# Kernel optimization log

Measured on AMD Instinct MI355X. Metric: run time of the kernel, lower is better.

Reference implementation:

```python
import jax, jax.numpy as jnp
import numpy as np

B, N, HID = 4, 1024, 256
NH, DH = 8, 32          # heads, head dim (HID = NH*DH)
BH = 64                 # bias MLP hidden


def setup_inputs() -> dict:
    key = jax.random.key(0)
    ks = jax.random.split(key, 12)
    s = lambda fan_in: 1.0 / np.sqrt(fan_in)
    return {
        "h": jax.random.normal(ks[0], (B, N, HID), jnp.float32),
        "coord": jax.random.uniform(ks[1], (B, N), jnp.float32),
        "mask": jnp.ones((B, N), jnp.int32),
        # qkv / proj linear params (stored [in, out])
        "Wqkv": jax.random.normal(ks[2], (HID, 3 * HID), jnp.float32) * s(HID),
        "bqkv": jnp.zeros((3 * HID,), jnp.float32),
        "Wproj": jax.random.normal(ks[3], (HID, HID), jnp.float32) * s(HID),
        "bproj": jnp.zeros((HID,), jnp.float32),
        # layernorm
        "gamma": jnp.ones((HID,), jnp.float32),
        "beta": jnp.zeros((HID,), jnp.float32),
        # relative-bias MLP: Linear(1->BH), SiLU, Linear(BH->BH), SiLU, Linear(BH->NH)
        "Wb1": jax.random.normal(ks[4], (1, BH), jnp.float32),
        "bb1": jnp.zeros((BH,), jnp.float32),
        "Wb2": jax.random.normal(ks[5], (BH, BH), jnp.float32) * s(BH),
        "bb2": jnp.zeros((BH,), jnp.float32),
        "Wb3": jax.random.normal(ks[6], (BH, NH), jnp.float32) * s(BH),
        "bb3": jnp.zeros((NH,), jnp.float32),
    }


def _layernorm(x, gamma, beta, eps=1e-5):
    mu = jnp.mean(x, axis=-1, keepdims=True)
    var = jnp.mean((x - mu) ** 2, axis=-1, keepdims=True)
    return (x - mu) * jax.lax.rsqrt(var + eps) * gamma + beta


def reference(h, coord, mask, Wqkv, bqkv, Wproj, bproj, gamma, beta,
              Wb1, bb1, Wb2, bb2, Wb3, bb3):
    x = _layernorm(h, gamma, beta)                      # [B,N,HID]
    qkv = x @ Wqkv + bqkv                               # [B,N,3*HID]
    q, k, v = jnp.split(qkv, 3, axis=-1)
    # [B,N,HID] -> [B,NH,N,DH]
    reshape = lambda t: t.reshape(B, N, NH, DH).transpose(0, 2, 1, 3)
    q, k, v = reshape(q), reshape(k), reshape(v)

    attn = jnp.einsum("bhqd,bhkd->bhqk", q, k) / np.sqrt(DH).astype(np.float32)

    # pairwise coordinate differences and learned bias
    dcoord = coord[:, None, :] - coord[:, :, None]      # [B,N,N]
    t = dcoord[..., None]                               # [B,N,N,1]
    t = jax.nn.silu(t @ Wb1 + bb1)                      # [B,N,N,BH]
    t = jax.nn.silu(t @ Wb2 + bb2)                      # [B,N,N,BH]
    bias = (t @ Wb3 + bb3)                              # [B,N,N,NH]
    attn = attn + bias.transpose(0, 3, 1, 2)            # [B,NH,N,N]

    neg_inf = jnp.array(-jnp.inf, attn.dtype)
    attn = jnp.where(mask[:, None, None, :] == 0, neg_inf, attn)
    w = jax.nn.softmax(attn, axis=-1)

    out = jnp.einsum("bhqk,bhkd->bhqd", w, v)           # [B,NH,N,DH]
    out = out.transpose(0, 2, 1, 3).reshape(B, N, HID)
    out = out @ Wproj + bproj
    return h + out
```

## Files before the change

### kernel.cpp

```cpp
#include <hip/hip_runtime.h>
#include <hip/hip_fp16.h>
#include <math.h>

#define BB   4
#define NN   1024
#define HIDD 256
#define NHD  8
#define DHD  32
#define BHD  64
#define TI2  2048
#define LOG2E 1.4426950408889634f

typedef __attribute__((ext_vector_type(8))) short bf16x8;
typedef __attribute__((ext_vector_type(4))) short bf16x4;
typedef __attribute__((ext_vector_type(4))) float f32x4;

__device__ __forceinline__ unsigned short f2bf(float x) {
  union { float f; unsigned u; } c; c.f = x;
  unsigned r = c.u + 0x7FFFu + ((c.u >> 16) & 1u);
  return (unsigned short)(r >> 16);
}
__device__ __forceinline__ float bf2f(unsigned short b) {
  union { unsigned u; float f; } c; c.u = ((unsigned)b) << 16;
  return c.f;
}

__device__ __forceinline__ void pv_mfma(f32x4& acc, bf16x4 a, bf16x4 b) {
#if __has_builtin(__builtin_amdgcn_mfma_f32_16x16x16bf16_1k)
  acc = __builtin_amdgcn_mfma_f32_16x16x16bf16_1k(a, b, acc, 0, 0, 0);
#else
  asm volatile("s_nop 1\n\t"
               "v_mfma_f32_16x16x16_bf16 %0, %1, %2, %0\n\t"
               "s_nop 7\n\t"
               "s_nop 3"
               : "+v"(acc) : "v"(a), "v"(b));
#endif
}

__global__ __launch_bounds__(256) void prep_kernel(
    const float* __restrict__ Wb1, const float* __restrict__ bb1,
    const float* __restrict__ Wb2, const float* __restrict__ bb2,
    const float* __restrict__ Wb3, const float* __restrict__ bb3,
    const float* __restrict__ Wqkv, const float* __restrict__ Wproj,
    unsigned* __restrict__ tblh, unsigned short* __restrict__ wtq,
    unsigned short* __restrict__ wtp)
{
  __shared__ float h1a[4][64], h1b[4][64], h2a[4][64], h2b[4][64];
  __shared__ float t[16][17];
  int bid = blockIdx.x, tid = threadIdx.x;
  if (bid < 512) {
    int g = tid >> 6, j = tid & 63;
    int pt = bid * 4 + g;
    float t0 = -1.0f + (float)pt     * (2.0f / (float)TI2);
    float t1 = -1.0f + (float)(pt+1) * (2.0f / (float)TI2);
    float w1 = Wb1[j], c1 = bb1[j];
    float z0 = fmaf(t0, w1, c1), z1 = fmaf(t1, w1, c1);
    h1a[g][j] = z0 / (1.0f + __expf(-z0));
    h1b[g][j] = z1 / (1.0f + __expf(-z1));
    __syncthreads();
    float a0 = bb2[j], a1 = a0;
    #pragma unroll 16
    for (int i = 0; i < BHD; ++i) {
      float wv = Wb2[i*BHD + j];
      a0 = fmaf(h1a[g][i], wv, a0);
      a1 = fmaf(h1b[g][i], wv, a1);
    }
    h2a[g][j] = a0 / (1.0f + __expf(-a0));
    h2b[g][j] = a1 / (1.0f + __expf(-a1));
    __syncthreads();
    if (j < NHD) {
      float o0 = bb3[j], o1 = o0;
      #pragma unroll 16
      for (int i = 0; i < BHD; ++i) {
        float wv = Wb3[i*NHD + j];
        o0 = fmaf(h2a[g][i], wv, o0);
        o1 = fmaf(h2b[g][i], wv, o1);
      }
      o0 *= LOG2E; o1 *= LOG2E;
      __half2 hh = __floats2half2_rn(o0, o1 - o0);
      tblh[j*TI2 + pt] = *(unsigned*)&hh;
    }
  } else {
    const float* W; unsigned short* Wt; int n0, k0, ncols;
    if (bid < 1280) {
      int rb = bid - 512;
      n0 = (rb % 48) * 16; k0 = (rb / 48) * 16; ncols = 768;
      W = Wqkv; Wt = wtq;
    } else {
      int rc = bid - 1280;
      n0 = (rc & 15) * 16; k0 = (rc >> 4) * 16; ncols = 256;
      W = Wproj; Wt = wtp;
    }
    int sx = tid & 15, sy = tid >> 4;
    t[sy][sx] = W[(size_t)(k0 + sy) * ncols + n0 + sx];
    __syncthreads();
    Wt[(size_t)(n0 + sy) * 256 + k0 + sx] = f2bf(t[sx][sy]);
  }
}

__global__ __launch_bounds__(256) void ln_qkv_mm_kernel(
    const float* __restrict__ h, const float* __restrict__ gamma,
    const float* __restrict__ beta, const unsigned short* __restrict__ Wt,
    const float* __restrict__ bqkv,
    unsigned short* __restrict__ qws, unsigned short* __restrict__ kws,
    unsigned short* __restrict__ vtws)
{
  __shared__ unsigned short xs[32][260];
  int tid = threadIdx.x;
  int m0 = blockIdx.x * 32, n0 = blockIdx.y * 128;

  {
    int r = tid >> 3, q = tid & 7;
    const float* hrow = h + (size_t)(m0 + r)*HIDD + q*32;
    float4 xv[8];
    float sum = 0.f, sq = 0.f;
    #pragma unroll
    for (int j = 0; j < 8; ++j) {
      xv[j] = *(const float4*)&hrow[j*4];
      sum += xv[j].x + xv[j].y + xv[j].z + xv[j].w;
      sq  += xv[j].x*xv[j].x + xv[j].y*xv[j].y + xv[j].z*xv[j].z + xv[j].w*xv[j].w;
    }
    sum += __shfl_xor(sum, 1); sq += __shfl_xor(sq, 1);
    sum += __shfl_xor(sum, 2); sq += __shfl_xor(sq, 2);
    sum += __shfl_xor(sum, 4); sq += __shfl_xor(sq, 4);
    float mu  = sum * (1.0f/HIDD);
    float var = sq  * (1.0f/HIDD) - mu*mu;
    float rs  = rsqrtf(var + 1e-5f);
    #pragma unroll
    for (int j2 = 0; j2 < 4; ++j2) {
      union { bf16x8 v; unsigned short u[8]; } o;
      #pragma unroll
      for (int e = 0; e < 2; ++e) {
        float4 x4 = xv[j2*2 + e];
        int col = q*32 + j2*8 + e*4;
        float4 gv = *(const float4*)&gamma[col];
        float4 bv = *(const float4*)&beta[col];
        o.u[e*4+0] = f2bf(fmaf((x4.x - mu)*rs, gv.x, bv.x));
        o.u[e*4+1] = f2bf(fmaf((x4.y - mu)*rs, gv.y, bv.y));
        o.u[e*4+2] = f2bf(fmaf((x4.z - mu)*rs, gv.z, bv.z));
        o.u[e*4+3] = f2bf(fmaf((x4.w - mu)*rs, gv.w, bv.w));
      }
      *(bf16x8*)&xs[r][q*32 + j2*8] = o.v;
    }
  }
  __syncthreads();

  int lane = tid & 63, w = tid >> 6;
  int lo = lane & 15, hi = lane >> 4;
  int rw = (w & 1) * 16;
  int cw = (w >> 1) * 64;
  f32x4 acc[4];
  #pragma unroll
  for (int nt = 0; nt < 4; ++nt) acc[nt] = (f32x4){0.f,0.f,0.f,0.f};

  #pragma unroll
  for (int ks = 0; ks < 8; ++ks) {
    bf16x8 af = *(const bf16x8*)&xs[rw + lo][ks*32 + hi*8];
    #pragma unroll
    for (int nt = 0; nt < 4; ++nt) {
      bf16x8 bf = *(const bf16x8*)&Wt[(size_t)(n0 + cw + nt*16 + lo)*256 + ks*32 + hi*8];
      acc[nt] = __builtin_amdgcn_mfma_f32_16x16x32_bf16(af, bf, acc[nt], 0, 0, 0);
    }
  }

  int m0w = m0 + rw;
  int b = m0w >> 10;
  if (n0 < 512) {
    unsigned short* dst = (n0 < 256) ? qws : kws;
    int nbase = (m0w & 1023) + hi*4;
    #pragma unroll
    for (int nt = 0; nt < 4; ++nt) {
      int c = n0 + cw + nt*16 + lo;
      int cr = c & 255;
      int head = cr >> 5, d = cr & 31;
      float bq = bqkv[c];
      size_t bh = (size_t)(b*NHD + head);
      #pragma unroll
      for (int r = 0; r < 4; ++r)
        dst[(bh*NN + nbase + r)*DHD + d] = f2bf(acc[nt][r] + bq);
    }
  } else {
    __syncthreads();
    unsigned short (*vt)[40] = (unsigned short(*)[40])&xs[0][0];
    #pragma unroll
    for (int nt = 0; nt < 4; ++nt) {
      int cr = cw + nt*16 + lo;
      float bq = bqkv[n0 + cr];
      union { unsigned short u[4]; unsigned wd[2]; } pk;
      #pragma unroll
      for (int r = 0; r < 4; ++r) pk.u[r] = f2bf(acc[nt][r] + bq);
      int col = rw + hi*4;
      *(unsigned*)&vt[cr][col]     = pk.wd[0];
      *(unsigned*)&vt[cr][col + 2] = pk.wd[1];
    }
    __syncthreads();
    int nn0 = m0 & 1023;
    #pragma unroll
    for (int i = 0; i < 2; ++i) {
      int u = i*256 + tid;
      int row = u >> 2, ch = u & 3;
      int cr256 = (n0 - 512) + row;
      int head = cr256 >> 5, d = cr256 & 31;
      *(bf16x8*)&vtws[((size_t)(b*NHD + head)*DHD + d)*NN + nn0 + ch*8] =
          *(const bf16x8*)&vt[row][ch*8];
    }
  }
}

__global__ __launch_bounds__(256, 4) void attn_kernel(
    const unsigned short* __restrict__ Q, const unsigned short* __restrict__ K,
    const unsigned short* __restrict__ Vt, const float* __restrict__ coord,
    const int* __restrict__ mask, const unsigned* __restrict__ tblh,
    unsigned short* __restrict__ pO, float2* __restrict__ pML)
{
  __shared__ unsigned tableL[TI2];
  __shared__ unsigned short Klds[2][64][40];
  __shared__ unsigned short Vtlds[2][32][72];

  int tid = threadIdx.x, lane = tid & 63, w = tid >> 6;
  int bh = blockIdx.y, half = blockIdx.z;
  int b = bh >> 3, head = bh & 7;
  int qbase = blockIdx.x * 64 + w * 16;
  int lo = lane & 15, hi = lane >> 4;

  for (int i = tid; i < TI2/4; i += 256)
    ((uint4*)tableL)[i] = ((const uint4*)(tblh + head*TI2))[i];

  bf16x8 qf = *(const bf16x8*)&Q[((size_t)bh*NN + qbase + lo)*DHD + hi*8];
  float qoff = fmaf(coord[b*NN + qbase + lo], -(float)TI2*0.5f, (float)TI2*0.5f);

  float m = -1e30f, l = 0.f;
  f32x4 oacc[2];
  oacc[0] = (f32x4){0.f,0.f,0.f,0.f};
  oacc[1] = (f32x4){0.f,0.f,0.f,0.f};
  const float scale2 = 0.17677669529663689f * LOG2E;

  int kt0 = half * (NN/2);
  int sr = tid >> 2, ss = tid & 3;
  int vr = tid >> 3, vs = tid & 7;
  {
    *(bf16x8*)&Klds[0][sr][ss*8] =
        *(const bf16x8*)&K[((size_t)bh*NN + kt0 + sr)*DHD + ss*8];
    *(bf16x8*)&Vtlds[0][vr][vs*8] =
        *(const bf16x8*)&Vt[((size_t)bh*DHD + vr)*NN + kt0 + vs*8];
  }
  __syncthreads();

  for (int t = 0; t < 8; ++t) {
    int kt = kt0 + t*64;
    int cur = t & 1;
    bf16x8 kn, vn;
    if (t < 7) {
      kn = *(const bf16x8*)&K[((size_t)bh*NN + kt + 64 + sr)*DHD + ss*8];
      vn = *(const bf16x8*)&Vt[((size_t)bh*DHD + vr)*NN + kt + 64 + vs*8];
    }
    float ck[4][4]; int mk[4][4];
    #pragma unroll
    for (int nt = 0; nt < 4; ++nt) {
      float4 c4 = *(const float4*)&coord[b*NN + kt + nt*16 + hi*4];
      int4   m4 = *(const int4*)  &mask [b*NN + kt + nt*16 + hi*4];
      ck[nt][0] = c4.x; ck[nt][1] = c4.y; ck[nt][2] = c4.z; ck[nt][3] = c4.w;
      mk[nt][0] = m4.x; mk[nt][1] = m4.y; mk[nt][2] = m4.z; mk[nt][3] = m4.w;
    }

    f32x4 z = {0.f,0.f,0.f,0.f};
    f32x4 sacc[4];
    #pragma unroll
    for (int nt = 0; nt < 4; ++nt) {
      bf16x8 kf = *(const bf16x8*)&Klds[cur][nt*16 + lo][hi*8];
      sacc[nt] = __builtin_amdgcn_mfma_f32_16x16x32_bf16(kf, qf, z, 0, 0, 0);
    }

    float sv[4][4];
    #pragma unroll
    for (int nt = 0; nt < 4; ++nt) {
      #pragma unroll
      for (int r = 0; r < 4; ++r) {
        float u = fmaf(ck[nt][r], (float)TI2*0.5f, qoff);
        u = fminf(fmaxf(u, 0.0f), (float)TI2 - 0.01f);
        int   i0 = (int)u;
        float fr = u - (float)i0;
        unsigned e = tableL[i0];
        __half2 hh = *(__half2*)&e;
        float bias = fmaf(__high2float(hh), fr, __low2float(hh));
        float s = fmaf(sacc[nt][r], scale2, bias);
        sv[nt][r] = mk[nt][r] ? s : -1e31f;
      }
    }

    float pm = sv[0][0];
    #pragma unroll
    for (int nt = 0; nt < 4; ++nt)
      #pragma unroll
      for (int r = 0; r < 4; ++r) pm = fmaxf(pm, sv[nt][r]);
    pm = fmaxf(pm, __shfl_xor(pm, 16));
    pm = fmaxf(pm, __shfl_xor(pm, 32));
    float mn = fmaxf(m, pm);
    if (mn > m) {
      float sf = __builtin_amdgcn_exp2f(m - mn);
      l *= sf;
      #pragma unroll
      for (int n2 = 0; n2 < 2; ++n2)
        #pragma unroll
        for (int r = 0; r < 4; ++r) oacc[n2][r] *= sf;
      m = mn;
    }

    bf16x4 pfrag[4];
    #pragma unroll
    for (int nt = 0; nt < 4; ++nt) {
      float p0 = __builtin_amdgcn_exp2f(sv[nt][0] - m);
      float p1 = __builtin_amdgcn_exp2f(sv[nt][1] - m);
      float p2 = __builtin_amdgcn_exp2f(sv[nt][2] - m);
      float p3 = __builtin_amdgcn_exp2f(sv[nt][3] - m);
      l += (p0 + p1) + (p2 + p3);
      union { bf16x4 v; unsigned short u[4]; } pk;
      pk.u[0] = f2bf(p0); pk.u[1] = f2bf(p1);
      pk.u[2] = f2bf(p2); pk.u[3] = f2bf(p3);
      pfrag[nt] = pk.v;
    }

    #pragma unroll
    for (int nt = 0; nt < 4; ++nt) {
      #pragma unroll
      for (int n2 = 0; n2 < 2; ++n2) {
        bf16x4 vf = *(const bf16x4*)&Vtlds[cur][n2*16 + lo][nt*16 + hi*4];
        pv_mfma(oacc[n2], vf, pfrag[nt]);
      }
    }

    if (t < 7) {
      *(bf16x8*)&Klds[cur^1][sr][ss*8] = kn;
      *(bf16x8*)&Vtlds[cur^1][vr][vs*8] = vn;
    }
    __syncthreads();
  }

  l += __shfl_xor(l, 16);
  l += __shfl_xor(l, 32);
  size_t base = ((size_t)(half*BB*NHD + bh)*NN + qbase + lo);
  #pragma unroll
  for (int n2 = 0; n2 < 2; ++n2) {
    union { bf16x4 v; unsigned short u[4]; } ov;
    ov.u[0] = f2bf(oacc[n2][0]); ov.u[1] = f2bf(oacc[n2][1]);
    ov.u[2] = f2bf(oacc[n2][2]); ov.u[3] = f2bf(oacc[n2][3]);
    *(bf16x4*)&pO[base*DHD + n2*16 + hi*4] = ov.v;
  }
  if (hi == 0) pML[base] = make_float2(m, l);
}

__global__ __launch_bounds__(128) void proj_mm_kernel(
    const unsigned short* __restrict__ pO, const float2* __restrict__ pML,
    const unsigned short* __restrict__ Wpt, const float* __restrict__ bp,
    const float* __restrict__ h, float* __restrict__ out)
{
  __shared__ unsigned short alds[32][264];
  int tid = threadIdx.x;
  int m0 = blockIdx.x * 32, n0 = blockIdx.y * 64;

  {
    int r = tid >> 2, q = tid & 3;
    int g = m0 + r, b = g >> 10, n = g & 1023;
    #pragma unroll
    for (int hh = 0; hh < 2; ++hh) {
      int hd = q*2 + hh;
      int bhh = b*NHD + hd;
      float2 ml0 = pML[(size_t)bhh*NN + n];
      float2 ml1 = pML[((size_t)(BB*NHD) + bhh)*NN + n];
      float mm = fmaxf(ml0.x, ml1.x);
      float e0 = __builtin_amdgcn_exp2f(ml0.x - mm);
      float e1 = __builtin_amdgcn_exp2f(ml1.x - mm);
      float inv = 1.0f / fmaf(ml0.y, e0, ml1.y * e1);
      e0 *= inv; e1 *= inv;
      const bf16x8* p0 = (const bf16x8*)&pO[((size_t)bhh*NN + n)*DHD];
      const bf16x8* p1 = (const bf16x8*)&pO[(((size_t)(BB*NHD) + bhh)*NN + n)*DHD];
      #pragma unroll
      for (int j = 0; j < 4; ++j) {
        union { bf16x8 v; unsigned short u[8]; } a, c, o;
        a.v = p0[j]; c.v = p1[j];
        #pragma unroll
        for (int e = 0; e < 8; ++e)
          o.u[e] = f2bf(fmaf(bf2f(a.u[e]), e0, bf2f(c.u[e]) * e1));
        *(bf16x8*)&alds[r][hd*32 + j*8] = o.v;
      }
    }
  }
  __syncthreads();

  int lane = tid & 63, w = tid >> 6;
  int lo = lane & 15, hi = lane >> 4;
  f32x4 acc[4];
  #pragma unroll
  for (int nt = 0; nt < 4; ++nt) acc[nt] = (f32x4){0.f,0.f,0.f,0.f};

  #pragma unroll
  for (int ks = 0; ks < 8; ++ks) {
    bf16x8 af = *(const bf16x8*)&alds[w*16 + lo][ks*32 + hi*8];
    #pragma unroll
    for (int nt = 0; nt < 4; ++nt) {
      bf16x8 bf = *(const bf16x8*)&Wpt[(size_t)(n0 + nt*16 + lo)*256 + ks*32 + hi*8];
      acc[nt] = __builtin_amdgcn_mfma_f32_16x16x32_bf16(af, bf, acc[nt], 0, 0, 0);
    }
  }

  int m0w = m0 + w*16;
  #pragma unroll
  for (int nt = 0; nt < 4; ++nt) {
    int c = n0 + nt*16 + lo;
    float bpv = bp[c];
    #pragma unroll
    for (int r = 0; r < 4; ++r) {
      size_t o = (size_t)(m0w + hi*4 + r)*HIDD + c;
      out[o] = h[o] + acc[nt][r] + bpv;
    }
  }
}

extern "C" void kernel_launch(void* const* d_in, const int* in_sizes, int n_in,
                              void* d_out, int out_size, void* d_ws, size_t ws_size,
                              hipStream_t stream)
{
  const float* h     = (const float*)d_in[0];
  const float* coord = (const float*)d_in[1];
  const int*   mask  = (const int*)  d_in[2];
  const float* Wqkv  = (const float*)d_in[3];
  const float* bqkv  = (const float*)d_in[4];
  const float* Wproj = (const float*)d_in[5];
  const float* bproj = (const float*)d_in[6];
  const float* gamma = (const float*)d_in[7];
  const float* beta  = (const float*)d_in[8];
  const float* Wb1   = (const float*)d_in[9];
  const float* bb1   = (const float*)d_in[10];
  const float* Wb2   = (const float*)d_in[11];
  const float* bb2   = (const float*)d_in[12];
  const float* Wb3   = (const float*)d_in[13];
  const float* bb3   = (const float*)d_in[14];
  float* out = (float*)d_out;

  unsigned* tblh = (unsigned*)d_ws;
  float2*   pML  = (float2*)(tblh + NHD*TI2);
  unsigned short* wtq  = (unsigned short*)(pML + (size_t)2*BB*NHD*NN);
  unsigned short* wtp  = wtq + 768*256;
  unsigned short* qws  = wtp + 256*256;
  unsigned short* kws  = qws + (size_t)BB*NHD*NN*DHD;
  unsigned short* vtws = kws + (size_t)BB*NHD*NN*DHD;
  unsigned short* pO   = vtws + (size_t)BB*NHD*NN*DHD;

  prep_kernel<<<dim3(1536), dim3(256), 0, stream>>>(
      Wb1, bb1, Wb2, bb2, Wb3, bb3, Wqkv, Wproj, tblh, wtq, wtp);
  ln_qkv_mm_kernel<<<dim3(BB*NN/32, 6), dim3(256), 0, stream>>>(
      h, gamma, beta, wtq, bqkv, qws, kws, vtws);
  attn_kernel<<<dim3(NN/64, BB*NHD, 2), dim3(256), 0, stream>>>(
      qws, kws, vtws, coord, mask, tblh, pO, pML);
  proj_mm_kernel<<<dim3(BB*NN/32, 4), dim3(128), 0, stream>>>(
      pO, pML, wtp, bproj, h, out);
}
```

Baseline: 67.12 us.

## Use nearest-neighbor bf16 bias table and split combine from projection GEMM

```diff
diff --git a/kernel.cpp b/kernel.cpp
--- a/kernel.cpp
+++ b/kernel.cpp
@@ -8,7 +8,8 @@
 #define NHD  8
 #define DHD  32
 #define BHD  64
-#define TI2  2048
+#define TI4  4096
+#define TBS  4104
 #define LOG2E 1.4426950408889634f
 
 typedef __attribute__((ext_vector_type(8))) short bf16x8;
@@ -42,52 +43,38 @@
     const float* __restrict__ Wb2, const float* __restrict__ bb2,
     const float* __restrict__ Wb3, const float* __restrict__ bb3,
     const float* __restrict__ Wqkv, const float* __restrict__ Wproj,
-    unsigned* __restrict__ tblh, unsigned short* __restrict__ wtq,
+    unsigned short* __restrict__ tblb, unsigned short* __restrict__ wtq,
     unsigned short* __restrict__ wtp)
 {
-  __shared__ float h1a[4][64], h1b[4][64], h2a[4][64], h2b[4][64];
+  __shared__ float h1a[4][64], h2a[4][64];
   __shared__ float t[16][17];
   int bid = blockIdx.x, tid = threadIdx.x;
-  if (bid < 512) {
+  if (bid < 1025) {
     int g = tid >> 6, j = tid & 63;
     int pt = bid * 4 + g;
-    float t0 = -1.0f + (float)pt     * (2.0f / (float)TI2);
-    float t1 = -1.0f + (float)(pt+1) * (2.0f / (float)TI2);
-    float w1 = Wb1[j], c1 = bb1[j];
-    float z0 = fmaf(t0, w1, c1), z1 = fmaf(t1, w1, c1);
+    float tt = -1.0f + (float)pt * (2.0f / (float)TI4);
+    float z0 = fmaf(tt, Wb1[j], bb1[j]);
     h1a[g][j] = z0 / (1.0f + __expf(-z0));
-    h1b[g][j] = z1 / (1.0f + __expf(-z1));
-    __syncthreads();
-    float a0 = bb2[j], a1 = a0;
+    __syncthreads();
+    float a0 = bb2[j];
     #pragma unroll 16
-    for (int i = 0; i < BHD; ++i) {
-      float wv = Wb2[i*BHD + j];
-      a0 = fmaf(h1a[g][i], wv, a0);
-      a1 = fmaf(h1b[g][i], wv, a1);
-    }
+    for (int i = 0; i < BHD; ++i) a0 = fmaf(h1a[g][i], Wb2[i*BHD + j], a0);
     h2a[g][j] = a0 / (1.0f + __expf(-a0));
-    h2b[g][j] = a1 / (1.0f + __expf(-a1));
-    __syncthreads();
-    if (j < NHD) {
-      float o0 = bb3[j], o1 = o0;
+    __syncthreads();
+    if (j < NHD && pt <= TI4) {
+      float o0 = bb3[j];
       #pragma unroll 16
-      for (int i = 0; i < BHD; ++i) {
-        float wv = Wb3[i*NHD + j];
-        o0 = fmaf(h2a[g][i], wv, o0);
-        o1 = fmaf(h2b[g][i], wv, o1);
-      }
-      o0 *= LOG2E; o1 *= LOG2E;
-      __half2 hh = __floats2half2_rn(o0, o1 - o0);
-      tblh[j*TI2 + pt] = *(unsigned*)&hh;
+      for (int i = 0; i < BHD; ++i) o0 = fmaf(h2a[g][i], Wb3[i*NHD + j], o0);
+      tblb[j*TBS + pt] = f2bf(o0 * LOG2E);
     }
   } else {
     const float* W; unsigned short* Wt; int n0, k0, ncols;
-    if (bid < 1280) {
-      int rb = bid - 512;
+    if (bid < 1793) {
+      int rb = bid - 1025;
       n0 = (rb % 48) * 16; k0 = (rb / 48) * 16; ncols = 768;
       W = Wqkv; Wt = wtq;
     } else {
-      int rc = bid - 1280;
+      int rc = bid - 1793;
       n0 = (rc & 15) * 16; k0 = (rc >> 4) * 16; ncols = 256;
       W = Wproj; Wt = wtp;
     }
@@ -210,10 +197,10 @@
 __global__ __launch_bounds__(256, 4) void attn_kernel(
     const unsigned short* __restrict__ Q, const unsigned short* __restrict__ K,
     const unsigned short* __restrict__ Vt, const float* __restrict__ coord,
-    const int* __restrict__ mask, const unsigned* __restrict__ tblh,
+    const int* __restrict__ mask, const unsigned short* __restrict__ tblb,
     unsigned short* __restrict__ pO, float2* __restrict__ pML)
 {
-  __shared__ unsigned tableL[TI2];
+  __shared__ unsigned short tableL[TBS];
   __shared__ unsigned short Klds[2][64][40];
   __shared__ unsigned short Vtlds[2][32][72];
 
@@ -223,11 +210,14 @@
   int qbase = blockIdx.x * 64 + w * 16;
   int lo = lane & 15, hi = lane >> 4;
 
-  for (int i = tid; i < TI2/4; i += 256)
-    ((uint4*)tableL)[i] = ((const uint4*)(tblh + head*TI2))[i];
+  {
+    const uint4* src = (const uint4*)(tblb + head*TBS);
+    uint4* dst = (uint4*)tableL;
+    for (int i = tid; i < TBS/8; i += 256) dst[i] = src[i];
+  }
 
   bf16x8 qf = *(const bf16x8*)&Q[((size_t)bh*NN + qbase + lo)*DHD + hi*8];
-  float qoff = fmaf(coord[b*NN + qbase + lo], -(float)TI2*0.5f, (float)TI2*0.5f);
+  float qoff2 = fmaf(coord[b*NN + qbase + lo], -(float)TI4*0.5f, (float)TI4*0.5f);
 
   float m = -1e30f, l = 0.f;
   f32x4 oacc[2];
@@ -276,13 +266,9 @@
     for (int nt = 0; nt < 4; ++nt) {
       #pragma unroll
       for (int r = 0; r < 4; ++r) {
-        float u = fmaf(ck[nt][r], (float)TI2*0.5f, qoff);
-        u = fminf(fmaxf(u, 0.0f), (float)TI2 - 0.01f);
-        int   i0 = (int)u;
-        float fr = u - (float)i0;
-        unsigned e = tableL[i0];
-        __half2 hh = *(__half2*)&e;
-        float bias = fmaf(__high2float(hh), fr, __low2float(hh));
+        float u = fmaf(ck[nt][r], (float)TI4*0.5f, qoff2);
+        int i0 = (int)(u + 0.5f);
+        float bias = bf2f(tableL[i0]);
         float s = fmaf(sacc[nt][r], scale2, bias);
         sv[nt][r] = mk[nt][r] ? s : -1e31f;
       }
@@ -349,68 +335,60 @@
   if (hi == 0) pML[base] = make_float2(m, l);
 }
 
-__global__ __launch_bounds__(128) void proj_mm_kernel(
+__global__ __launch_bounds__(256) void combine_kernel(
     const unsigned short* __restrict__ pO, const float2* __restrict__ pML,
-    const unsigned short* __restrict__ Wpt, const float* __restrict__ bp,
-    const float* __restrict__ h, float* __restrict__ out)
-{
-  __shared__ unsigned short alds[32][264];
-  int tid = threadIdx.x;
-  int m0 = blockIdx.x * 32, n0 = blockIdx.y * 64;
-
-  {
-    int r = tid >> 2, q = tid & 3;
-    int g = m0 + r, b = g >> 10, n = g & 1023;
-    #pragma unroll
-    for (int hh = 0; hh < 2; ++hh) {
-      int hd = q*2 + hh;
-      int bhh = b*NHD + hd;
-      float2 ml0 = pML[(size_t)bhh*NN + n];
-      float2 ml1 = pML[((size_t)(BB*NHD) + bhh)*NN + n];
-      float mm = fmaxf(ml0.x, ml1.x);
-      float e0 = __builtin_amdgcn_exp2f(ml0.x - mm);
-      float e1 = __builtin_amdgcn_exp2f(ml1.x - mm);
-      float inv = 1.0f / fmaf(ml0.y, e0, ml1.y * e1);
-      e0 *= inv; e1 *= inv;
-      const bf16x8* p0 = (const bf16x8*)&pO[((size_t)bhh*NN + n)*DHD];
-      const bf16x8* p1 = (const bf16x8*)&pO[(((size_t)(BB*NHD) + bhh)*NN + n)*DHD];
-      #pragma unroll
-      for (int j = 0; j < 4; ++j) {
-        union { bf16x8 v; unsigned short u[8]; } a, c, o;
-        a.v = p0[j]; c.v = p1[j];
-        #pragma unroll
-        for (int e = 0; e < 8; ++e)
-          o.u[e] = f2bf(fmaf(bf2f(a.u[e]), e0, bf2f(c.u[e]) * e1));
-        *(bf16x8*)&alds[r][hd*32 + j*8] = o.v;
-      }
-    }
-  }
-  __syncthreads();
-
-  int lane = tid & 63, w = tid >> 6;
+    unsigned short* __restrict__ aob)
+{
+  int idx = blockIdx.x * 256 + threadIdx.x;
+  int rg = idx >> 2, d8 = (idx & 3) << 3;
+  int bh = rg >> 10, n = rg & 1023;
+  int b = bh >> 3, head = bh & 7;
+  float2 ml0 = pML[rg];
+  float2 ml1 = pML[(size_t)(BB*NHD)*NN + rg];
+  float mm = fmaxf(ml0.x, ml1.x);
+  float e0 = __builtin_amdgcn_exp2f(ml0.x - mm);
+  float e1 = __builtin_amdgcn_exp2f(ml1.x - mm);
+  float inv = 1.0f / fmaf(ml0.y, e0, ml1.y * e1);
+  e0 *= inv; e1 *= inv;
+  union { bf16x8 v; unsigned short u[8]; } a, c, o;
+  a.v = *(const bf16x8*)&pO[(size_t)rg*DHD + d8];
+  c.v = *(const bf16x8*)&pO[((size_t)(BB*NHD)*NN + rg)*DHD + d8];
+  #pragma unroll
+  for (int e = 0; e < 8; ++e)
+    o.u[e] = f2bf(fmaf(bf2f(a.u[e]), e0, bf2f(c.u[e]) * e1));
+  *(bf16x8*)&aob[((size_t)(b*NN + n))*HIDD + head*DHD + d8] = o.v;
+}
+
+__global__ __launch_bounds__(256) void proj_mm_kernel(
+    const unsigned short* __restrict__ AO, const unsigned short* __restrict__ Wpt,
+    const float* __restrict__ bp, const float* __restrict__ h,
+    float* __restrict__ out)
+{
+  int tid = threadIdx.x, lane = tid & 63, w = tid >> 6;
   int lo = lane & 15, hi = lane >> 4;
-  f32x4 acc[4];
-  #pragma unroll
-  for (int nt = 0; nt < 4; ++nt) acc[nt] = (f32x4){0.f,0.f,0.f,0.f};
+  int m0 = blockIdx.x * 32 + (w & 1) * 16;
+  int n0 = blockIdx.y * 64 + (w >> 1) * 32;
+  f32x4 acc[2];
+  acc[0] = (f32x4){0.f,0.f,0.f,0.f};
+  acc[1] = (f32x4){0.f,0.f,0.f,0.f};
 
   #pragma unroll
   for (int ks = 0; ks < 8; ++ks) {
-    bf16x8 af = *(const bf16x8*)&alds[w*16 + lo][ks*32 + hi*8];
-    #pragma unroll
-    for (int nt = 0; nt < 4; ++nt) {
+    bf16x8 af = *(const bf16x8*)&AO[(size_t)(m0 + lo)*256 + ks*32 + hi*8];
+    #pragma unroll
+    for (int nt = 0; nt < 2; ++nt) {
       bf16x8 bf = *(const bf16x8*)&Wpt[(size_t)(n0 + nt*16 + lo)*256 + ks*32 + hi*8];
       acc[nt] = __builtin_amdgcn_mfma_f32_16x16x32_bf16(af, bf, acc[nt], 0, 0, 0);
     }
   }
 
-  int m0w = m0 + w*16;
-  #pragma unroll
-  for (int nt = 0; nt < 4; ++nt) {
+  #pragma unroll
+  for (int nt = 0; nt < 2; ++nt) {
     int c = n0 + nt*16 + lo;
     float bpv = bp[c];
     #pragma unroll
     for (int r = 0; r < 4; ++r) {
-      size_t o = (size_t)(m0w + hi*4 + r)*HIDD + c;
+      size_t o = (size_t)(m0 + hi*4 + r)*HIDD + c;
       out[o] = h[o] + acc[nt][r] + bpv;
     }
   }
@@ -437,21 +415,23 @@
   const float* bb3   = (const float*)d_in[14];
   float* out = (float*)d_out;
 
-  unsigned* tblh = (unsigned*)d_ws;
-  float2*   pML  = (float2*)(tblh + NHD*TI2);
+  unsigned short* tblb = (unsigned short*)d_ws;
+  float2* pML = (float2*)(tblb + NHD*TBS);
   unsigned short* wtq  = (unsigned short*)(pML + (size_t)2*BB*NHD*NN);
   unsigned short* wtp  = wtq + 768*256;
   unsigned short* qws  = wtp + 256*256;
   unsigned short* kws  = qws + (size_t)BB*NHD*NN*DHD;
   unsigned short* vtws = kws + (size_t)BB*NHD*NN*DHD;
   unsigned short* pO   = vtws + (size_t)BB*NHD*NN*DHD;
-
-  prep_kernel<<<dim3(1536), dim3(256), 0, stream>>>(
-      Wb1, bb1, Wb2, bb2, Wb3, bb3, Wqkv, Wproj, tblh, wtq, wtp);
+  unsigned short* aob  = pO + (size_t)2*BB*NHD*NN*DHD;
+
+  prep_kernel<<<dim3(2049), dim3(256), 0, stream>>>(
+      Wb1, bb1, Wb2, bb2, Wb3, bb3, Wqkv, Wproj, tblb, wtq, wtp);
   ln_qkv_mm_kernel<<<dim3(BB*NN/32, 6), dim3(256), 0, stream>>>(
       h, gamma, beta, wtq, bqkv, qws, kws, vtws);
   attn_kernel<<<dim3(NN/64, BB*NHD, 2), dim3(256), 0, stream>>>(
-      qws, kws, vtws, coord, mask, tblh, pO, pML);
-  proj_mm_kernel<<<dim3(BB*NN/32, 4), dim3(128), 0, stream>>>(
-      pO, pML, wtp, bproj, h, out);
-}
+      qws, kws, vtws, coord, mask, tblb, pO, pML);
+  combine_kernel<<<dim3(512), dim3(256), 0, stream>>>(pO, pML, aob);
+  proj_mm_kernel<<<dim3(BB*NN/32, 4), dim3(256), 0, stream>>>(
+      aob, wtp, bproj, h, out);
+}
```

Result: no change. 67.22 us (+0.1%).
